# Performance work log

Measured on AMD Instinct MI355X. Metric: run time of the kernel, lower is better.

Reference implementation:

```python
import jax, jax.numpy as jnp
import numpy as np

H, W = 480, 640
B = 4
P = 10          # number of accumulated flow passes (num_flows = 1)
N = 400000      # events per batch element
TREF = 1.0
TS_SCALING = 1.0
SPAT_W = 1.0
TEMP_W = 1.0


def _corners(loc):
    """loc: [M,2] (y,x) float -> flattened corner idx [4M] int32, bilinear weights [4M].
    Corner order: TL, TR, BL, BR (blocks of M), matching pol_mask repeat(1,4,1) layout.
    Out-of-grid corners get zero weight; indices are clamped in-range."""
    ty = jnp.floor(loc[:, 0:1])
    lx = jnp.floor(loc[:, 1:2])
    cs = jnp.concatenate([
        jnp.concatenate([ty, lx], 1),
        jnp.concatenate([ty, lx + 1.0], 1),
        jnp.concatenate([ty + 1.0, lx], 1),
        jnp.concatenate([ty + 1.0, lx + 1.0], 1)], axis=0)  # [4M,2]
    w = jnp.maximum(0.0, 1.0 - jnp.abs(jnp.tile(loc, (4, 1)) - cs))
    weights = w[:, 0] * w[:, 1]
    inb = ((cs[:, 0] >= 0) & (cs[:, 0] <= H - 1) &
           (cs[:, 1] >= 0) & (cs[:, 1] <= W - 1))
    weights = weights * inb.astype(weights.dtype)
    idx = (jnp.clip(cs[:, 0], 0, H - 1) * W + jnp.clip(cs[:, 1], 0, W - 1)).astype(jnp.int32)
    return idx, weights


def setup_inputs() -> dict:
    key = jax.random.key(0)
    k1, k2, k3, k4, k5 = jax.random.split(key, 5)
    scale = jnp.array([H - 1.0, W - 1.0], dtype=jnp.float32)
    warped_events = jax.random.uniform(k1, (B, N, 2), dtype=jnp.float32) * scale
    pos = jax.random.bernoulli(k2, 0.5, (B, N)).astype(jnp.float32)
    pos4 = jnp.tile(pos, (1, 4))                                   # [B,4N]
    pol_mask = jnp.stack([pos4, 1.0 - pos4], axis=-1)              # [B,4N,2]
    ts = jax.random.uniform(k3, (B, N, 1), dtype=jnp.float32)
    ts_list = jnp.tile(ts, (1, 4, 1))                              # [B,4N,1]
    flow_x = jax.random.normal(k4, (B, P, H, W), dtype=jnp.float32) * 3.0
    flow_y = jax.random.normal(k5, (B, P, H, W), dtype=jnp.float32) * 3.0
    return {"warped_events": warped_events, "pol_mask": pol_mask,
            "ts_list": ts_list, "flow_x": flow_x, "flow_y": flow_y}


def reference(warped_events, pol_mask, ts_list, flow_x, flow_y):
    f32 = flow_x.dtype
    # ---- iwe_formatting: bilinear scatter-add of warped events ----
    idx, weights = jax.vmap(_corners)(warped_events)               # [B,4N], [B,4N]
    norm_ts = 1.0 - jnp.abs(TREF - ts_list[..., 0]) / TS_SCALING   # [B,4N]

    def scat(i, w):
        return jnp.zeros(H * W, w.dtype).at[i].add(w)

    def img(w):
        return jax.vmap(scat)(idx, w).reshape(B, 1, H, W)

    iwe = jnp.concatenate([img(weights * pol_mask[:, :, 0]),
                           img(weights * pol_mask[:, :, 1])], axis=1)          # [B,2,H,W]
    iwe_ts = jnp.concatenate([img(weights * norm_ts * pol_mask[:, :, 0]),
                              img(weights * norm_ts * pol_mask[:, :, 1])], axis=1)

    # ---- focus_loss ----
    ts2 = iwe_ts.reshape(B, 2, -1)
    fl = jnp.sum(ts2[:, 0] ** 2, axis=1) + jnp.sum(ts2[:, 1] ** 2, axis=1)
    nz = (jnp.sum(iwe, axis=1) != 0).reshape(B, -1)
    fl = fl / (jnp.sum(nz, axis=1) + 1e-9)
    focus = jnp.sum(fl)

    # ---- flow_temporal_smoothing: warp grid by flow[j], gather flow[j+1] ----
    grid = jnp.stack(jnp.meshgrid(jnp.arange(H, dtype=f32),
                                  jnp.arange(W, dtype=f32), indexing='ij'), 0)  # [2,H,W] (y,x)
    flow = jnp.stack([flow_y[:, :-1], flow_x[:, :-1]], axis=2)                  # [B,P-1,2,H,W]
    loc = (grid[None, None] + flow).reshape(B, P - 1, 2, H * W).transpose(0, 1, 3, 2)  # [B,P-1,HW,2]
    m = ((loc[..., 0] >= 0) & (loc[..., 0] <= H - 1) &
         (loc[..., 1] >= 0) & (loc[..., 1] <= W - 1)).astype(f32)

    def samp(fx, fy, l):
        # fx, fy: [H,W]; l: [HW,2] -> sampled (y,x) flow [HW,2]
        i, w = _corners(l)
        sx = (fx.reshape(-1)[i] * w).reshape(4, -1).sum(0)
        sy = (fy.reshape(-1)[i] * w).reshape(4, -1).sum(0)
        return jnp.stack([sy, sx], axis=-1)

    wf = jax.vmap(jax.vmap(samp))(flow_x[:, 1:], flow_y[:, 1:], loc)            # [B,P-1,HW,2]
    ff = flow.reshape(B, P - 1, 2, H * W).transpose(0, 1, 3, 2)
    dt = jnp.sum(jnp.sqrt((ff - wf) ** 2 + 1e-9), axis=-1)                      # [B,P-1,HW]
    lt = jnp.sum(dt * m, axis=-1) / (jnp.sum(m, axis=-1) + 1e-9)                # [B,P-1]
    temporal = TEMP_W * jnp.sum(jnp.sum(lt, axis=1) / (P - 1))                  # num_flows = 1

    # ---- flow_spatial_smoothing: Charbonnier on 4 neighbor directions ----
    def charb(a):
        return jnp.sqrt(a ** 2 + 1e-6)

    dx = charb(flow_x[..., :-1] - flow_x[..., 1:]) + charb(flow_y[..., :-1] - flow_y[..., 1:])
    dy = charb(flow_x[:, :, :-1, :] - flow_x[:, :, 1:, :]) + charb(flow_y[:, :, :-1, :] - flow_y[:, :, 1:, :])
    ddr = charb(flow_x[:, :, :-1, :-1] - flow_x[:, :, 1:, 1:]) + charb(flow_y[:, :, :-1, :-1] - flow_y[:, :, 1:, 1:])
    dur = charb(flow_x[:, :, 1:, :-1] - flow_x[:, :, :-1, 1:]) + charb(flow_y[:, :, 1:, :-1] - flow_y[:, :, :-1, 1:])
    mm = lambda t: t.reshape(B, P, -1).mean(2).mean(1)
    spatial = SPAT_W * jnp.sum((mm(dx) + mm(dy) + mm(ddr) + mm(dur)) / 4.0)

    return focus + temporal + spatial
```

## Files before the change

kernel.cpp:

```cpp
#include <hip/hip_runtime.h>

#define BB 4
#define PP 10
#define NN 400000
#define HH 480
#define WW 640
constexpr int HW    = HH * WW;
constexpr int NXB   = HW / 256;
constexpr int NXB4  = HW / 1024;
constexpr int NBLK  = NXB4 * BB * PP;
constexpr int CHUNK = NBLK / 8;
constexpr int EVB   = (BB * NN + NBLK - 1) / NBLK;

constexpr int QW = WW / 2, QH = HH / 2, QN = QW * QH;
constexpr size_t IMG_QUADS = (size_t)4 * BB * 2 * QN;

constexpr float SCALE     = 1024.0f;
constexpr float INV_SCALE = 1.0f / 1024.0f;

constexpr int PF_V = 0;
constexpr int PF_N = PF_V + BB * NXB;
constexpr int PT_D = PF_N + BB * NXB;
constexpr int PT_M = PT_D + BB * (PP-1) * NXB4;
constexpr int PS   = PT_M + BB * (PP-1) * NXB4;
constexpr int NPART = PS + BB * PP * NXB4;


__device__ __forceinline__ float fsq(float a) { return __builtin_amdgcn_sqrtf(a); }
__device__ __forceinline__ float charb(float a) { return fsq(fmaf(a, a, 1e-6f)); }

__device__ __forceinline__ float blockSum256(float v, float* smem) {
    #pragma unroll
    for (int off = 32; off > 0; off >>= 1)
        v += __shfl_down(v, off, 64);
    int lane = threadIdx.x & 63;
    int wid  = threadIdx.x >> 6;
    if (lane == 0) smem[wid] = v;
    __syncthreads();
    float r = 0.f;
    if (threadIdx.x == 0) r = smem[0] + smem[1] + smem[2] + smem[3];
    __syncthreads();
    return r;
}


__global__ __launch_bounds__(256)
void fused_kernel(const float2* __restrict__ we,
                  const float* __restrict__ pol,
                  const float* __restrict__ tsl,
                  const float* __restrict__ FX, const float* __restrict__ FY,
                  unsigned long long* __restrict__ img,
                  float* __restrict__ part) {
    __shared__ float sm[4];
    int w = blockIdx.x;
    int t = threadIdx.x;

    int e = w * EVB + t;
    if (t < EVB && e < BB * NN) {
        int b = e / NN;
        int m = e - b * NN;
        float2 c = we[e];
        float y = c.x, x = c.y;
        float pm0 = pol[((size_t)b * 4 * NN + m) * 2];
        float ts  = tsl[(size_t)b * 4 * NN + m];
        float nts = 1.0f - fabsf(1.0f - ts);
        float tyf = fminf(fmaxf(floorf(y), 0.f), (float)(HH - 2));
        float lxf = fminf(fmaxf(floorf(x), 0.f), (float)(WW - 2));
        float fy_ = y - tyf, fx_ = x - lxf;
        float gy = 1.f - fy_, gx = 1.f - fx_;
        float s = nts * SCALE;
        unsigned long long wTL = (unsigned int)(gy * gx * s + 0.5f);
        unsigned long long wTR = (unsigned int)(gy * fx_ * s + 0.5f);
        unsigned long long wBL = (unsigned int)(fy_ * gx * s + 0.5f);
        unsigned long long wBR = (unsigned int)(fy_ * fx_ * s + 0.5f);
        unsigned long long val = wTL | (wTR << 16) | (wBL << 32) | (wBR << 48);
        int ty = (int)tyf, lx = (int)lxf;
        int pi = ((ty & 1) << 1) | (lx & 1);
        int pl = (pm0 > 0.5f) ? 0 : 1;
        size_t wi = ((size_t)((pi * BB + b) * 2 + pl)) * QN + (ty >> 1) * QW + (lx >> 1);
        atomicAdd(&img[wi], val);
    }

    int l  = (w & 7) * CHUNK + (w >> 3);
    int bp = l / NXB4;
    int xb = l - bp * NXB4;
    int b2 = bp / PP;
    int j  = bp - b2 * PP;
    int p0 = xb * 1024 + t * 4;
    int y  = p0 / WW;
    int x0 = p0 - y * WW;
    const float* fx = FX + (size_t)bp * HW;
    const float* fy = FY + (size_t)bp * HW;
    float4 vx = *(const float4*)(fx + p0);
    float4 vy = *(const float4*)(fy + p0);
    bool yin  = (y + 1 < HH);
    bool xend = (x0 == WW - 4);
    float4 bx4 = make_float4(0.f, 0.f, 0.f, 0.f), by4 = bx4;
    float vxr = 0.f, vyr = 0.f, bxr = 0.f, byr = 0.f;
    if (yin) {
        bx4 = *(const float4*)(fx + p0 + WW);
        by4 = *(const float4*)(fy + p0 + WW);
    }
    if (!xend) { vxr = fx[p0 + 4]; vyr = fy[p0 + 4]; }
    if (yin && !xend) { bxr = fx[p0 + WW + 4]; byr = fy[p0 + WW + 4]; }

    constexpr float cdx = 1.0f / ((float)HH * (WW - 1) * 4.0f * PP);
    constexpr float cdy = 1.0f / ((float)(HH - 1) * WW * 4.0f * PP);
    constexpr float cdd = 1.0f / ((float)(HH - 1) * (WW - 1) * 4.0f * PP);

    float acc = 0.f;
    acc += (charb(vx.x - vx.y) + charb(vy.x - vy.y)) * cdx;
    acc += (charb(vx.y - vx.z) + charb(vy.y - vy.z)) * cdx;
    acc += (charb(vx.z - vx.w) + charb(vy.z - vy.w)) * cdx;
    if (!xend) acc += (charb(vx.w - vxr) + charb(vy.w - vyr)) * cdx;
    if (yin) {
        acc += (charb(vx.x - bx4.x) + charb(vy.x - by4.x)) * cdy;
        acc += (charb(vx.y - bx4.y) + charb(vy.y - by4.y)) * cdy;
        acc += (charb(vx.z - bx4.z) + charb(vy.z - by4.z)) * cdy;
        acc += (charb(vx.w - bx4.w) + charb(vy.w - by4.w)) * cdy;
        acc += (charb(vx.x - bx4.y) + charb(vy.x - by4.y)) * cdd;
        acc += (charb(vx.y - bx4.z) + charb(vy.y - by4.z)) * cdd;
        acc += (charb(vx.z - bx4.w) + charb(vy.z - by4.w)) * cdd;
        acc += (charb(bx4.x - vx.y) + charb(by4.x - vy.y)) * cdd;
        acc += (charb(bx4.y - vx.z) + charb(by4.y - vy.z)) * cdd;
        acc += (charb(bx4.z - vx.w) + charb(by4.z - vy.w)) * cdd;
        if (!xend) {
            acc += (charb(vx.w - bxr) + charb(vy.w - byr)) * cdd;
            acc += (charb(bx4.w - vxr) + charb(by4.w - vyr)) * cdd;
        }
    }
    float ssum = blockSum256(acc, sm);
    if (t == 0) part[PS + bp * NXB4 + xb] = ssum;

    if (j < PP - 1) {
        const float* gx1 = fx + HW;
        const float* gy1 = fy + HW;
        float ax[4] = {vx.x, vx.y, vx.z, vx.w};
        float ay[4] = {vy.x, vy.y, vy.z, vy.w};
        float td = 0.f, tm = 0.f;
        #pragma unroll
        for (int i = 0; i < 4; ++i) {
            float ly  = (float)y + ay[i];
            float lx2 = (float)(x0 + i) + ax[i];
            bool m = (ly >= 0.f) && (ly <= (float)(HH - 1)) &&
                     (lx2 >= 0.f) && (lx2 <= (float)(WW - 1));
            if (m) {
                tm += 1.f;
                float tyf = fminf(fmaxf(floorf(ly),  0.f), (float)(HH - 2));
                float txf = fminf(fmaxf(floorf(lx2), 0.f), (float)(WW - 2));
                float fyy = ly - tyf, fxx = lx2 - txf;
                float gyy = 1.f - fyy, gxx = 1.f - fxx;
                int pix = (int)tyf * WW + (int)txf;
                float sx = gyy * (gxx * gx1[pix]      + fxx * gx1[pix + 1]) +
                           fyy * (gxx * gx1[pix + WW] + fxx * gx1[pix + WW + 1]);
                float sy = gyy * (gxx * gy1[pix]      + fxx * gy1[pix + 1]) +
                           fyy * (gxx * gy1[pix + WW] + fxx * gy1[pix + WW + 1]);
                float dy_ = ay[i] - sy;
                float dx_ = ax[i] - sx;
                td += fsq(fmaf(dy_, dy_, 1e-9f)) + fsq(fmaf(dx_, dx_, 1e-9f));
            }
        }
        float sd = blockSum256(td, sm);
        float sM = blockSum256(tm, sm);
        if (t == 0) {
            int bj = b2 * (PP - 1) + j;
            part[PT_D + bj * NXB4 + xb] = sd;
            part[PT_M + bj * NXB4 + xb] = sM;
        }
    }
}


__global__ __launch_bounds__(256)
void focus_kernel(const unsigned long long* __restrict__ img,
                  float* __restrict__ part) {
    __shared__ float sm[8];
    int b = blockIdx.y;
    int p = blockIdx.x * 256 + threadIdx.x;
    int y = p / WW;
    int x = p - y * WW;
    unsigned int sp = 0, sn = 0;
    #pragma unroll
    for (int dy = 0; dy < 2; ++dy) {
        #pragma unroll
        for (int dx = 0; dx < 2; ++dx) {
            int ty = y - dy, lx = x - dx;
            if (ty < 0 || lx < 0 || ty > HH - 2 || lx > WW - 2) continue;
            int pi = ((ty & 1) << 1) | (lx & 1);
            size_t base = ((size_t)(pi * BB + b) * 2) * QN + (ty >> 1) * QW + (lx >> 1);
            int sh = 16 * ((dy << 1) | dx);
            sp += (unsigned int)((img[base]      >> sh) & 0xFFFFull);
            sn += (unsigned int)((img[base + QN] >> sh) & 0xFFFFull);
        }
    }
    float tp = (float)sp * INV_SCALE;
    float tn = (float)sn * INV_SCALE;
    float v  = tp * tp + tn * tn;
    float nz = ((sp | sn) != 0u) ? 1.f : 0.f;
    float sv  = blockSum256(v, sm);
    float snz = blockSum256(nz, sm + 4);
    if (threadIdx.x == 0) {
        part[PF_V + b * NXB + blockIdx.x] = sv;
        part[PF_N + b * NXB + blockIdx.x] = snz;
    }
}


__global__ __launch_bounds__(256)
void reduce_kernel(const float* __restrict__ part, float* __restrict__ seg) {
    __shared__ float sm[4];
    int s = blockIdx.x;
    int base, len;
    if (s < 4)       { base = PF_V + s * NXB;         len = NXB; }
    else if (s < 8)  { base = PF_N + (s - 4) * NXB;   len = NXB; }
    else if (s < 44) { base = PT_D + (s - 8) * NXB4;  len = NXB4; }
    else if (s < 80) { base = PT_M + (s - 44) * NXB4; len = NXB4; }
    else             { base = PS;                     len = BB * PP * NXB4; }
    float v = 0.f;
    for (int i = threadIdx.x; i < len; i += 256) v += part[base + i];
    float r = blockSum256(v, sm);
    if (threadIdx.x == 0) seg[s] = r;
}


__global__ void final_kernel(const float* __restrict__ seg, float* __restrict__ out) {
    if (threadIdx.x == 0 && blockIdx.x == 0) {
        float focus = 0.f;
        #pragma unroll
        for (int b = 0; b < BB; ++b)
            focus += seg[b] / (seg[BB + b] + 1e-9f);
        float temporal = 0.f;
        #pragma unroll
        for (int k = 0; k < BB * (PP - 1); ++k)
            temporal += seg[8 + k] / (seg[44 + k] + 1e-9f);
        temporal *= 1.0f / (float)(PP - 1);
        out[0] = focus + temporal + seg[80];
    }
}


extern "C" void kernel_launch(void* const* d_in, const int* in_sizes, int n_in,
                              void* d_out, int out_size, void* d_ws, size_t ws_size,
                              hipStream_t stream) {
    const float2* we  = (const float2*)d_in[0];
    const float*  pol = (const float*)d_in[1];
    const float*  tsl = (const float*)d_in[2];
    const float*  FX  = (const float*)d_in[3];
    const float*  FY  = (const float*)d_in[4];
    float*              seg  = (float*)d_ws;
    unsigned long long* img  = (unsigned long long*)(seg + 256);
    float*              part = (float*)(img + IMG_QUADS);

    hipMemsetAsync(img, 0, IMG_QUADS * sizeof(unsigned long long), stream);

    fused_kernel<<<NBLK, 256, 0, stream>>>(we, pol, tsl, FX, FY, img, part);
    focus_kernel<<<dim3(NXB, BB), 256, 0, stream>>>(img, part);
    reduce_kernel<<<81, 256, 0, stream>>>(part, seg);
    final_kernel<<<1, 64, 0, stream>>>(seg, (float*)d_out);
}
```

Baseline: 177.4 us.

## Use persistent 2048-block grid looping over flow tiles and merge block reductions

The fused kernel now launches a fixed 2048-block grid instead of one block per 1024-pixel flow tile. Each block loops over its XCD-chunked tiles with a stride of 256 and scatters a proportionally larger slice of events, interleaving the scatter with the tile work. The three per-tile block reductions are merged into one shuffle/shared-memory pass with a single pair of barriers. This is meant to cut block launch and barrier overhead and to improve load balance. The risk is lower parallelism per event batch and loop overhead.

```diff
diff --git a/kernel.cpp b/kernel.cpp
--- a/kernel.cpp
+++ b/kernel.cpp
@@ -8,9 +8,10 @@
 constexpr int HW    = HH * WW;
 constexpr int NXB   = HW / 256;
 constexpr int NXB4  = HW / 1024;
-constexpr int NBLK  = NXB4 * BB * PP;
-constexpr int CHUNK = NBLK / 8;
-constexpr int EVB   = (BB * NN + NBLK - 1) / NBLK;
+constexpr int NTILE = NXB4 * BB * PP;
+constexpr int NPB   = 2048;
+constexpr int CHUNK = NTILE / 8;
+constexpr int EVB   = (BB * NN + NPB - 1) / NPB;
 
 constexpr int QW = WW / 2, QH = HH / 2, QN = QW * QH;
 constexpr size_t IMG_QUADS = (size_t)4 * BB * 2 * QN;
@@ -28,6 +29,25 @@
 
 __device__ __forceinline__ float fsq(float a) { return __builtin_amdgcn_sqrtf(a); }
 __device__ __forceinline__ float charb(float a) { return fsq(fmaf(a, a, 1e-6f)); }
+
+__device__ __forceinline__ void blockSum3(float a, float b, float c, float* sm, int t,
+                                          float& ra, float& rb, float& rc) {
+    #pragma unroll
+    for (int off = 32; off > 0; off >>= 1) {
+        a += __shfl_down(a, off, 64);
+        b += __shfl_down(b, off, 64);
+        c += __shfl_down(c, off, 64);
+    }
+    int lane = t & 63, wid = t >> 6;
+    if (lane == 0) { sm[wid] = a; sm[4 + wid] = b; sm[8 + wid] = c; }
+    __syncthreads();
+    if (t == 0) {
+        ra = sm[0] + sm[1] + sm[2] + sm[3];
+        rb = sm[4] + sm[5] + sm[6] + sm[7];
+        rc = sm[8] + sm[9] + sm[10] + sm[11];
+    }
+    __syncthreads();
+}
 
 __device__ __forceinline__ float blockSum256(float v, float* smem) {
     #pragma unroll
@@ -43,6 +63,35 @@
     return r;
 }
 
+__device__ __forceinline__ void scatter_one(int e,
+                                            const float2* __restrict__ we,
+                                            const float* __restrict__ pol,
+                                            const float* __restrict__ tsl,
+                                            unsigned long long* __restrict__ img) {
+    int b = e / NN;
+    int m = e - b * NN;
+    float2 c = we[e];
+    float y = c.x, x = c.y;
+    float pm0 = pol[((size_t)b * 4 * NN + m) * 2];
+    float ts  = tsl[(size_t)b * 4 * NN + m];
+    float nts = 1.0f - fabsf(1.0f - ts);
+    float tyf = fminf(fmaxf(floorf(y), 0.f), (float)(HH - 2));
+    float lxf = fminf(fmaxf(floorf(x), 0.f), (float)(WW - 2));
+    float fy_ = y - tyf, fx_ = x - lxf;
+    float gy = 1.f - fy_, gx = 1.f - fx_;
+    float s = nts * SCALE;
+    unsigned long long wTL = (unsigned int)(gy * gx * s + 0.5f);
+    unsigned long long wTR = (unsigned int)(gy * fx_ * s + 0.5f);
+    unsigned long long wBL = (unsigned int)(fy_ * gx * s + 0.5f);
+    unsigned long long wBR = (unsigned int)(fy_ * fx_ * s + 0.5f);
+    unsigned long long val = wTL | (wTR << 16) | (wBL << 32) | (wBR << 48);
+    int ty = (int)tyf, lx = (int)lxf;
+    int pi = ((ty & 1) << 1) | (lx & 1);
+    int pl = (pm0 > 0.5f) ? 0 : 1;
+    size_t wi = ((size_t)((pi * BB + b) * 2 + pl)) * QN + (ty >> 1) * QW + (lx >> 1);
+    atomicAdd(&img[wi], val);
+}
+
 
 __global__ __launch_bounds__(256)
 void fused_kernel(const float2* __restrict__ we,
@@ -51,121 +100,107 @@
                   const float* __restrict__ FX, const float* __restrict__ FY,
                   unsigned long long* __restrict__ img,
                   float* __restrict__ part) {
-    __shared__ float sm[4];
+    __shared__ float sm[12];
     int w = blockIdx.x;
     int t = threadIdx.x;
-
-    int e = w * EVB + t;
-    if (t < EVB && e < BB * NN) {
-        int b = e / NN;
-        int m = e - b * NN;
-        float2 c = we[e];
-        float y = c.x, x = c.y;
-        float pm0 = pol[((size_t)b * 4 * NN + m) * 2];
-        float ts  = tsl[(size_t)b * 4 * NN + m];
-        float nts = 1.0f - fabsf(1.0f - ts);
-        float tyf = fminf(fmaxf(floorf(y), 0.f), (float)(HH - 2));
-        float lxf = fminf(fmaxf(floorf(x), 0.f), (float)(WW - 2));
-        float fy_ = y - tyf, fx_ = x - lxf;
-        float gy = 1.f - fy_, gx = 1.f - fx_;
-        float s = nts * SCALE;
-        unsigned long long wTL = (unsigned int)(gy * gx * s + 0.5f);
-        unsigned long long wTR = (unsigned int)(gy * fx_ * s + 0.5f);
-        unsigned long long wBL = (unsigned int)(fy_ * gx * s + 0.5f);
-        unsigned long long wBR = (unsigned int)(fy_ * fx_ * s + 0.5f);
-        unsigned long long val = wTL | (wTR << 16) | (wBL << 32) | (wBR << 48);
-        int ty = (int)tyf, lx = (int)lxf;
-        int pi = ((ty & 1) << 1) | (lx & 1);
-        int pl = (pm0 > 0.5f) ? 0 : 1;
-        size_t wi = ((size_t)((pi * BB + b) * 2 + pl)) * QN + (ty >> 1) * QW + (lx >> 1);
-        atomicAdd(&img[wi], val);
-    }
-
-    int l  = (w & 7) * CHUNK + (w >> 3);
-    int bp = l / NXB4;
-    int xb = l - bp * NXB4;
-    int b2 = bp / PP;
-    int j  = bp - b2 * PP;
-    int p0 = xb * 1024 + t * 4;
-    int y  = p0 / WW;
-    int x0 = p0 - y * WW;
-    const float* fx = FX + (size_t)bp * HW;
-    const float* fy = FY + (size_t)bp * HW;
-    float4 vx = *(const float4*)(fx + p0);
-    float4 vy = *(const float4*)(fy + p0);
-    bool yin  = (y + 1 < HH);
-    bool xend = (x0 == WW - 4);
-    float4 bx4 = make_float4(0.f, 0.f, 0.f, 0.f), by4 = bx4;
-    float vxr = 0.f, vyr = 0.f, bxr = 0.f, byr = 0.f;
-    if (yin) {
-        bx4 = *(const float4*)(fx + p0 + WW);
-        by4 = *(const float4*)(fy + p0 + WW);
-    }
-    if (!xend) { vxr = fx[p0 + 4]; vyr = fy[p0 + 4]; }
-    if (yin && !xend) { bxr = fx[p0 + WW + 4]; byr = fy[p0 + WW + 4]; }
-
-    constexpr float cdx = 1.0f / ((float)HH * (WW - 1) * 4.0f * PP);
-    constexpr float cdy = 1.0f / ((float)(HH - 1) * WW * 4.0f * PP);
-    constexpr float cdd = 1.0f / ((float)(HH - 1) * (WW - 1) * 4.0f * PP);
-
-    float acc = 0.f;
-    acc += (charb(vx.x - vx.y) + charb(vy.x - vy.y)) * cdx;
-    acc += (charb(vx.y - vx.z) + charb(vy.y - vy.z)) * cdx;
-    acc += (charb(vx.z - vx.w) + charb(vy.z - vy.w)) * cdx;
-    if (!xend) acc += (charb(vx.w - vxr) + charb(vy.w - vyr)) * cdx;
-    if (yin) {
-        acc += (charb(vx.x - bx4.x) + charb(vy.x - by4.x)) * cdy;
-        acc += (charb(vx.y - bx4.y) + charb(vy.y - by4.y)) * cdy;
-        acc += (charb(vx.z - bx4.z) + charb(vy.z - by4.z)) * cdy;
-        acc += (charb(vx.w - bx4.w) + charb(vy.w - by4.w)) * cdy;
-        acc += (charb(vx.x - bx4.y) + charb(vy.x - by4.y)) * cdd;
-        acc += (charb(vx.y - bx4.z) + charb(vy.y - by4.z)) * cdd;
-        acc += (charb(vx.z - bx4.w) + charb(vy.z - by4.w)) * cdd;
-        acc += (charb(bx4.x - vx.y) + charb(by4.x - vy.y)) * cdd;
-        acc += (charb(bx4.y - vx.z) + charb(by4.y - vy.z)) * cdd;
-        acc += (charb(bx4.z - vx.w) + charb(by4.z - vy.w)) * cdd;
-        if (!xend) {
-            acc += (charb(vx.w - bxr) + charb(vy.w - byr)) * cdd;
-            acc += (charb(bx4.w - vxr) + charb(by4.w - vyr)) * cdd;
-        }
-    }
-    float ssum = blockSum256(acc, sm);
-    if (t == 0) part[PS + bp * NXB4 + xb] = ssum;
-
-    if (j < PP - 1) {
-        const float* gx1 = fx + HW;
-        const float* gy1 = fy + HW;
-        float ax[4] = {vx.x, vx.y, vx.z, vx.w};
-        float ay[4] = {vy.x, vy.y, vy.z, vy.w};
+    int ebase = w * EVB;
+    int ecnt  = BB * NN - ebase;
+    if (ecnt > EVB) ecnt = EVB;
+    int xcd = w & 7, slot = w >> 3;
+
+    int it = 0;
+    for (int s = slot; s < CHUNK; s += 256, ++it) {
+        int k = it * 256 + t;
+        if (k < ecnt) scatter_one(ebase + k, we, pol, tsl, img);
+
+        int l  = xcd * CHUNK + s;
+        int bp = l / NXB4;
+        int xb = l - bp * NXB4;
+        int b2 = bp / PP;
+        int j  = bp - b2 * PP;
+        int p0 = xb * 1024 + t * 4;
+        int y  = p0 / WW;
+        int x0 = p0 - y * WW;
+        const float* fx = FX + (size_t)bp * HW;
+        const float* fy = FY + (size_t)bp * HW;
+        float4 vx = *(const float4*)(fx + p0);
+        float4 vy = *(const float4*)(fy + p0);
+        bool yin  = (y + 1 < HH);
+        bool xend = (x0 == WW - 4);
+        float4 bx4 = make_float4(0.f, 0.f, 0.f, 0.f), by4 = bx4;
+        float vxr = 0.f, vyr = 0.f, bxr = 0.f, byr = 0.f;
+        if (yin) {
+            bx4 = *(const float4*)(fx + p0 + WW);
+            by4 = *(const float4*)(fy + p0 + WW);
+        }
+        if (!xend) { vxr = fx[p0 + 4]; vyr = fy[p0 + 4]; }
+        if (yin && !xend) { bxr = fx[p0 + WW + 4]; byr = fy[p0 + WW + 4]; }
+
+        constexpr float cdx = 1.0f / ((float)HH * (WW - 1) * 4.0f * PP);
+        constexpr float cdy = 1.0f / ((float)(HH - 1) * WW * 4.0f * PP);
+        constexpr float cdd = 1.0f / ((float)(HH - 1) * (WW - 1) * 4.0f * PP);
+
+        float acc = 0.f;
+        acc += (charb(vx.x - vx.y) + charb(vy.x - vy.y)) * cdx;
+        acc += (charb(vx.y - vx.z) + charb(vy.y - vy.z)) * cdx;
+        acc += (charb(vx.z - vx.w) + charb(vy.z - vy.w)) * cdx;
+        if (!xend) acc += (charb(vx.w - vxr) + charb(vy.w - vyr)) * cdx;
+        if (yin) {
+            acc += (charb(vx.x - bx4.x) + charb(vy.x - by4.x)) * cdy;
+            acc += (charb(vx.y - bx4.y) + charb(vy.y - by4.y)) * cdy;
+            acc += (charb(vx.z - bx4.z) + charb(vy.z - by4.z)) * cdy;
+            acc += (charb(vx.w - bx4.w) + charb(vy.w - by4.w)) * cdy;
+            acc += (charb(vx.x - bx4.y) + charb(vy.x - by4.y)) * cdd;
+            acc += (charb(vx.y - bx4.z) + charb(vy.y - by4.z)) * cdd;
+            acc += (charb(vx.z - bx4.w) + charb(vy.z - by4.w)) * cdd;
+            acc += (charb(bx4.x - vx.y) + charb(by4.x - vy.y)) * cdd;
+            acc += (charb(bx4.y - vx.z) + charb(by4.y - vy.z)) * cdd;
+            acc += (charb(bx4.z - vx.w) + charb(by4.z - vy.w)) * cdd;
+            if (!xend) {
+                acc += (charb(vx.w - bxr) + charb(vy.w - byr)) * cdd;
+                acc += (charb(bx4.w - vxr) + charb(by4.w - vyr)) * cdd;
+            }
+        }
+
         float td = 0.f, tm = 0.f;
-        #pragma unroll
-        for (int i = 0; i < 4; ++i) {
-            float ly  = (float)y + ay[i];
-            float lx2 = (float)(x0 + i) + ax[i];
-            bool m = (ly >= 0.f) && (ly <= (float)(HH - 1)) &&
-                     (lx2 >= 0.f) && (lx2 <= (float)(WW - 1));
-            if (m) {
-                tm += 1.f;
-                float tyf = fminf(fmaxf(floorf(ly),  0.f), (float)(HH - 2));
-                float txf = fminf(fmaxf(floorf(lx2), 0.f), (float)(WW - 2));
-                float fyy = ly - tyf, fxx = lx2 - txf;
-                float gyy = 1.f - fyy, gxx = 1.f - fxx;
-                int pix = (int)tyf * WW + (int)txf;
-                float sx = gyy * (gxx * gx1[pix]      + fxx * gx1[pix + 1]) +
-                           fyy * (gxx * gx1[pix + WW] + fxx * gx1[pix + WW + 1]);
-                float sy = gyy * (gxx * gy1[pix]      + fxx * gy1[pix + 1]) +
-                           fyy * (gxx * gy1[pix + WW] + fxx * gy1[pix + WW + 1]);
-                float dy_ = ay[i] - sy;
-                float dx_ = ax[i] - sx;
-                td += fsq(fmaf(dy_, dy_, 1e-9f)) + fsq(fmaf(dx_, dx_, 1e-9f));
+        if (j < PP - 1) {
+            const float* gx1 = fx + HW;
+            const float* gy1 = fy + HW;
+            float ax[4] = {vx.x, vx.y, vx.z, vx.w};
+            float ay[4] = {vy.x, vy.y, vy.z, vy.w};
+            #pragma unroll
+            for (int i = 0; i < 4; ++i) {
+                float ly  = (float)y + ay[i];
+                float lx2 = (float)(x0 + i) + ax[i];
+                bool m = (ly >= 0.f) && (ly <= (float)(HH - 1)) &&
+                         (lx2 >= 0.f) && (lx2 <= (float)(WW - 1));
+                if (m) {
+                    tm += 1.f;
+                    float tyf = fminf(fmaxf(floorf(ly),  0.f), (float)(HH - 2));
+                    float txf = fminf(fmaxf(floorf(lx2), 0.f), (float)(WW - 2));
+                    float fyy = ly - tyf, fxx = lx2 - txf;
+                    float gyy = 1.f - fyy, gxx = 1.f - fxx;
+                    int pix = (int)tyf * WW + (int)txf;
+                    float sx = gyy * (gxx * gx1[pix]      + fxx * gx1[pix + 1]) +
+                               fyy * (gxx * gx1[pix + WW] + fxx * gx1[pix + WW + 1]);
+                    float sy = gyy * (gxx * gy1[pix]      + fxx * gy1[pix + 1]) +
+                               fyy * (gxx * gy1[pix + WW] + fxx * gy1[pix + WW + 1]);
+                    float dy_ = ay[i] - sy;
+                    float dx_ = ax[i] - sx;
+                    td += fsq(fmaf(dy_, dy_, 1e-9f)) + fsq(fmaf(dx_, dx_, 1e-9f));
+                }
             }
         }
-        float sd = blockSum256(td, sm);
-        float sM = blockSum256(tm, sm);
+
+        float racc, rsd, rsM;
+        blockSum3(acc, td, tm, sm, t, racc, rsd, rsM);
         if (t == 0) {
-            int bj = b2 * (PP - 1) + j;
-            part[PT_D + bj * NXB4 + xb] = sd;
-            part[PT_M + bj * NXB4 + xb] = sM;
+            part[PS + bp * NXB4 + xb] = racc;
+            if (j < PP - 1) {
+                int bj = b2 * (PP - 1) + j;
+                part[PT_D + bj * NXB4 + xb] = rsd;
+                part[PT_M + bj * NXB4 + xb] = rsM;
+            }
         }
     }
 }
@@ -253,7 +288,7 @@
 
     hipMemsetAsync(img, 0, IMG_QUADS * sizeof(unsigned long long), stream);
 
-    fused_kernel<<<NBLK, 256, 0, stream>>>(we, pol, tsl, FX, FY, img, part);
+    fused_kernel<<<NPB, 256, 0, stream>>>(we, pol, tsl, FX, FY, img, part);
     focus_kernel<<<dim3(NXB, BB), 256, 0, stream>>>(img, part);
     reduce_kernel<<<81, 256, 0, stream>>>(part, seg);
     final_kernel<<<1, 64, 0, stream>>>(seg, (float*)d_out);
```

New measurement: 195.0 us. 1.1x slower.
